# Optimization experiments

Hardware: AMD Instinct MI355X
Metric: run time of the kernel (lower is better)

## Reference

```python
import jax, jax.numpy as jnp
import numpy as np

DIM = 2048
H = 16
KV_RANK = 512
NOPE = 128
ROPE_D = 64
VD = 128
QK = NOPE + ROPE_D  # 192
SCALE = QK ** -0.5
B, S = 2, 2048
EPS = 1e-5


def _rope(x, start_pos):
    # x: (b, s, h, d) or (b, s, d); rotate along last dim, positions along axis 1
    s = x.shape[1]
    d = x.shape[-1]
    half = d // 2
    inv_freq = 1.0 / (10000.0 ** (jnp.arange(half, dtype=jnp.float32) * (2.0 / d)))
    pos = jnp.arange(start_pos, start_pos + s, dtype=jnp.float32)
    ang = pos[:, None] * inv_freq[None, :]  # (s, half)
    cos, sin = jnp.cos(ang), jnp.sin(ang)
    if x.ndim == 4:
        cos, sin = cos[None, :, None, :], sin[None, :, None, :]
    else:
        cos, sin = cos[None, :, :], sin[None, :, :]
    x1, x2 = x[..., :half], x[..., half:]
    return jnp.concatenate([x1 * cos - x2 * sin, x2 * cos + x1 * sin], axis=-1).astype(x.dtype)


def _layernorm(x, w, b):
    mu = jnp.mean(x, axis=-1, keepdims=True)
    var = jnp.mean(jnp.square(x - mu), axis=-1, keepdims=True)
    return (x - mu) * jax.lax.rsqrt(var + EPS) * w + b


def setup_inputs() -> dict:
    key = jax.random.key(0)
    ks = jax.random.split(key, 6)
    std = 0.02
    x = jax.random.normal(ks[0], (B, S, DIM), dtype=jnp.float32)
    wq = jax.random.normal(ks[1], (H * QK, DIM), dtype=jnp.float32) * std
    wkv_a = jax.random.normal(ks[2], (KV_RANK + ROPE_D, DIM), dtype=jnp.float32) * std
    wkv_b = jax.random.normal(ks[3], (H * (NOPE + VD), KV_RANK), dtype=jnp.float32) * std
    wo = jax.random.normal(ks[4], (DIM, H * VD), dtype=jnp.float32) * std
    kv_norm_w = jnp.ones((KV_RANK,), dtype=jnp.float32)
    kv_norm_b = jnp.zeros((KV_RANK,), dtype=jnp.float32)
    return {"x": x, "wq": wq, "wkv_a": wkv_a, "kv_norm_w": kv_norm_w,
            "kv_norm_b": kv_norm_b, "wkv_b": wkv_b, "wo": wo, "start_pos": 0}


def reference(x, wq, wkv_a, kv_norm_w, kv_norm_b, wkv_b, wo, start_pos):
    b, s, _ = x.shape
    # query projection: (b,s,H,QK)
    q = (x @ wq.T).reshape(b, s, H, QK)
    q_nope, q_pe = q[..., :NOPE], q[..., NOPE:]
    q_pe = _rope(q_pe, start_pos)
    # compressed kv + rope key
    kv_all = x @ wkv_a.T                      # (b,s,KV_RANK+ROPE_D)
    kv, k_pe = kv_all[..., :KV_RANK], kv_all[..., KV_RANK:]
    k_pe = _rope(k_pe, start_pos)             # (b,s,ROPE_D)
    kvn = _layernorm(kv, kv_norm_w, kv_norm_b)  # (b,s,KV_RANK)
    # absorb path: expand compressed kv through per-head wkv_b blocks
    w = wkv_b.reshape(H, NOPE + VD, KV_RANK)
    k_nope = jnp.einsum('btc,hdc->bthd', kvn, w[:, :NOPE])   # (b,t,H,NOPE)
    v = jnp.einsum('btc,hdc->bthd', kvn, w[:, NOPE:])        # (b,t,H,VD)
    q_full = jnp.concatenate([q_nope, q_pe], axis=-1)        # (b,s,H,QK)
    k_full = jnp.concatenate(
        [k_nope, jnp.broadcast_to(k_pe[:, :, None, :], (b, s, H, ROPE_D))], axis=-1)
    scores = jnp.einsum('bshd,bthd->bhst', q_full, k_full) * SCALE
    causal = jnp.tril(jnp.ones((s, s), dtype=bool))
    scores = jnp.where(causal[None, None], scores, jnp.float32(-1e30))
    attn = jax.nn.softmax(scores, axis=-1)
    out = jnp.einsum('bhst,bthd->bshd', attn, v).reshape(b, s, H * VD)
    return out @ wo.T
```

## Files before the change

kernel.cpp:

```cpp
#include <hip/hip_runtime.h>
#include <hip/hip_bf16.h>
#include <math.h>

typedef __bf16 bf16_t;
typedef __bf16 bf16x2 __attribute__((ext_vector_type(2)));
typedef __bf16 bf16x4 __attribute__((ext_vector_type(4)));
typedef __bf16 bf16x8 __attribute__((ext_vector_type(8)));
typedef float f32x4 __attribute__((ext_vector_type(4)));

#define SEQ 2048
#define MLA_SCALE 0.07216878364870322f
#define LN_EPS 1e-5f

__device__ __forceinline__ void gload_lds16(const bf16_t* g, bf16_t* l) {
    __builtin_amdgcn_global_load_lds(
        (const __attribute__((address_space(1))) uint32_t*)(const void*)g,
        (__attribute__((address_space(3))) uint32_t*)(void*)l, 16, 0, 0);
}

__device__ __forceinline__ void xcd_map(int bid, int total, int nbn,
                                        int& bm, int& bn) {
    int per = total >> 3;
    int cbm = per / nbn;
    int xcd = bid & 7, s = bid >> 3;
    int q = s / nbn;
    bm = xcd * cbm + q;
    bn = s - q * nbn;
}

#define CVT_N0 2097152
#define CVT_N1 1572864
#define CVT_N2 294912
#define CVT_N3 524288
#define CVT_N4 1048576
#define CVT_TOT (CVT_N0 + CVT_N1 + CVT_N2 + CVT_N3 + CVT_N4)

__global__ __launch_bounds__(256)
void cvt_all(const float* __restrict__ x, const float* __restrict__ wq,
             const float* __restrict__ wa, const float* __restrict__ wb,
             const float* __restrict__ wo, bf16_t* __restrict__ xb,
             bf16_t* __restrict__ wqb, bf16_t* __restrict__ wab,
             bf16_t* __restrict__ wbb, bf16_t* __restrict__ wob) {
    for (int i = blockIdx.x * 256 + threadIdx.x; i < CVT_TOT; i += gridDim.x * 256) {
        const float* src; bf16_t* dst; int off = i;
        if (i < CVT_N0) { src = x; dst = xb; }
        else if (i < CVT_N0 + CVT_N1) { src = wq; dst = wqb; off = i - CVT_N0; }
        else if (i < CVT_N0 + CVT_N1 + CVT_N2) { src = wa; dst = wab; off = i - CVT_N0 - CVT_N1; }
        else if (i < CVT_N0 + CVT_N1 + CVT_N2 + CVT_N3) { src = wb; dst = wbb; off = i - CVT_N0 - CVT_N1 - CVT_N2; }
        else { src = wo; dst = wob; off = i - CVT_N0 - CVT_N1 - CVT_N2 - CVT_N3; }
        float4 v = ((const float4*)src)[off];
        bf16x4 p = { (bf16_t)v.x, (bf16_t)v.y, (bf16_t)v.z, (bf16_t)v.w };
        ((bf16x4*)dst)[off] = p;
    }
}

#define G256_PHASE(TAU, KS, MH, HTO, MAT, WAITV)                               \
{                                                                              \
    const int slot_ = (2 * (TAU) + (KS)) & 3;                                  \
    bf16x8 af_[4];                                                             \
    {                                                                          \
        const bf16_t* ab_ = As + slot_ * 8192 +                                \
                            (wm2 * 128 + (MH) * 64 + lr) * 32 + rdcol;         \
        _Pragma("unroll")                                                      \
        for (int f = 0; f < 4; ++f) af_[f] = *(const bf16x8*)(ab_ + f * 512);  \
    }                                                                          \
    if ((MH) == 0) {                                                           \
        const bf16_t* bb_ = Bs + slot_ * 8192 + (wn2 * 64 + lr) * 32 + rdcol;  \
        _Pragma("unroll")                                                      \
        for (int f = 0; f < 4; ++f) bq[f] = *(const bf16x8*)(bb_ + f * 512);   \
    }                                                                          \
    if ((MAT) == 0) stageA(2 * T + 3 + (HTO)); else stageB(2 * T + 3 + (HTO)); \
    __builtin_amdgcn_s_barrier();                                              \
    asm volatile("" ::: "memory");                                             \
    __builtin_amdgcn_s_setprio(1);                                             \
    _Pragma("unroll")                                                          \
    for (int f = 0; f < 4; ++f)                                                \
        _Pragma("unroll")                                                      \
        for (int n = 0; n < 4; ++n)                                            \
            acc[(MH) * 4 + f][n] = __builtin_amdgcn_mfma_f32_16x16x32_bf16(    \
                af_[f], bq[n], acc[(MH) * 4 + f][n], 0, 0, 0);                 \
    __builtin_amdgcn_s_setprio(0);                                             \
    asm volatile("" ::: "memory");                                             \
    if (WAITV) asm volatile("s_waitcnt vmcnt(8)" ::: "memory");                \
    __builtin_amdgcn_s_barrier();                                              \
}

template<int MODE>
__global__ __launch_bounds__(512, 2)
void gemm256(const bf16_t* __restrict__ A, const bf16_t* __restrict__ B,
             float* __restrict__ C, bf16_t* __restrict__ out0,
             bf16_t* __restrict__ out1, int N, int K, int total, int nbn) {
    __shared__ __attribute__((aligned(16))) bf16_t As[32768];
    __shared__ __attribute__((aligned(16))) bf16_t Bs[32768];
    __shared__ __attribute__((aligned(16))) bf16_t Ds[8192];

    const int tid = threadIdx.x;
    const int lane = tid & 63, w = tid >> 6;
    const int lr = lane & 15, kh = lane >> 4;
    const int wm2 = w >> 2, wn2 = w & 3;
    int bm, bn;
    xcd_map(blockIdx.x, total, nbn, bm, bn);
    const int NT = K >> 6;

    const int rdcol = 8 * (kh ^ ((lr >> 1) & 3));
    const int strow = (w << 5) + (lane >> 2);
    const int scol = 8 * ((lane & 3) ^ ((lane >> 3) & 3));

    f32x4 acc[8][4];
    #pragma unroll
    for (int i = 0; i < 8; ++i)
        #pragma unroll
        for (int j = 0; j < 4; ++j) acc[i][j] = 0.0f;

    auto stageA = [&](int ht) {
        int hs = (ht < 2 * NT) ? ht : (2 * NT - 1);
        int tau = hs >> 1, kap = hs & 1;
        const bf16_t* g = A + (size_t)(bm * 256 + strow) * K + tau * 64 + kap * 32 + scol;
        bf16_t* l = (ht < 2 * NT) ? (As + (ht & 3) * 8192 + w * 1024) : (Ds + w * 1024);
        gload_lds16(g, l);
        gload_lds16(g + (size_t)16 * K, l + 512);
    };
    auto stageB = [&](int ht) {
        int hs = (ht < 2 * NT) ? ht : (2 * NT - 1);
        int tau = hs >> 1, kap = hs & 1;
        const bf16_t* g = B + (size_t)(bn * 256 + strow) * K + tau * 64 + kap * 32 + scol;
        bf16_t* l = (ht < 2 * NT) ? (Bs + (ht & 3) * 8192 + w * 1024) : (Ds + w * 1024);
        gload_lds16(g, l);
        gload_lds16(g + (size_t)16 * K, l + 512);
    };

    stageA(0); stageB(0); stageA(1); stageB(1); stageA(2); stageB(2);
    asm volatile("s_waitcnt vmcnt(8)" ::: "memory");
    __builtin_amdgcn_s_barrier();

    for (int it = 0; it < (NT >> 1); ++it) {
        const int T = 2 * it;
        bf16x8 bq[4];
        G256_PHASE(T,     0, 0, 0, 0, 0)
        G256_PHASE(T,     0, 1, 0, 1, 1)
        G256_PHASE(T,     1, 0, 1, 0, 0)
        G256_PHASE(T,     1, 1, 1, 1, 1)
        G256_PHASE(T + 1, 0, 0, 2, 0, 0)
        G256_PHASE(T + 1, 0, 1, 2, 1, 1)
        G256_PHASE(T + 1, 1, 0, 3, 0, 0)
        G256_PHASE(T + 1, 1, 1, 3, 1, 1)
    }

    const int rg = kh * 4;
    if (MODE == 0) {
        #pragma unroll
        for (int mf = 0; mf < 8; ++mf)
            #pragma unroll
            for (int nf = 0; nf < 4; ++nf) {
                size_t row0 = (size_t)(bm * 256 + wm2 * 128 + mf * 16 + rg);
                int col = bn * 256 + wn2 * 64 + nf * 16 + lr;
                #pragma unroll
                for (int rr = 0; rr < 4; ++rr)
                    C[(row0 + rr) * N + col] = acc[mf][nf][rr];
            }
    } else if (MODE == 1) {
        const int h = bn;
        #pragma unroll
        for (int mf = 0; mf < 8; ++mf)
            #pragma unroll
            for (int nf = 0; nf < 4; ++nf) {
                int d = wn2 * 64 + nf * 16 + lr;
                int trow = bm * 256 + wm2 * 128 + mf * 16 + rg;
                int b = trow >> 11, t = trow & 2047;
                if (d < 128) {
                    bf16_t* p = out0 + ((size_t)(b * 16 + h) * SEQ + t) * 192 + d;
                    #pragma unroll
                    for (int rr = 0; rr < 4; ++rr)
                        p[rr * 192] = (bf16_t)acc[mf][nf][rr];
                } else {
                    bf16x4 pv = { (bf16_t)acc[mf][nf][0], (bf16_t)acc[mf][nf][1],
                                  (bf16_t)acc[mf][nf][2], (bf16_t)acc[mf][nf][3] };
                    *(bf16x4*)(out1 + ((size_t)(b * 16 + h) * 128 + (d - 128)) * SEQ + t) = pv;
                }
            }
    } else {
        #pragma unroll
        for (int mf = 0; mf < 8; ++mf)
            #pragma unroll
            for (int nf = 0; nf < 4; ++nf) {
                int n = bn * 256 + wn2 * 64 + nf * 16 + lr;
                int h = n / 192, d = n - h * 192;
                int trow = bm * 256 + wm2 * 128 + mf * 16 + rg;
                int b = trow >> 11, t = trow & 2047;
                bf16_t* p = out0 + ((size_t)(b * 16 + h) * SEQ + t) * 192 + d;
                #pragma unroll
                for (int rr = 0; rr < 4; ++rr)
                    p[rr * 192] = (bf16_t)acc[mf][nf][rr];
            }
    }
}

__global__ __launch_bounds__(256)
void gemm_nt(const bf16_t* __restrict__ A, const bf16_t* __restrict__ B,
             float* __restrict__ C, int M, int N, int K, int total, int nbn) {
    __shared__ bf16_t As[4096], Bs[4096];
    int bm, bn;
    xcd_map(blockIdx.x, total, nbn, bm, bn);

    const int tid = threadIdx.x;
    const int lane = tid & 63, w = tid >> 6;
    const int lr = lane & 15, kh = lane >> 4;
    const int wm = (w >> 1) * 64, wn = (w & 1) * 64;
    const int subrow = lane >> 2;
    const int colel = (lane & 3) * 8;

    f32x4 acc[4][4];
    #pragma unroll
    for (int i = 0; i < 4; ++i)
        #pragma unroll
        for (int j = 0; j < 4; ++j) acc[i][j] = 0.0f;

    const int rA = bm * 128 + 32 * w + subrow;
    const int rB = bn * 128 + 32 * w + subrow;
    const int rb1 = (rB < N) ? rB : (N - 1);
    const int rb2 = (rB + 16 < N) ? (rB + 16) : (N - 1);

    for (int kt = 0; kt < K; kt += 32) {
        __syncthreads();
        gload_lds16(A + (size_t)rA * K + kt + colel,        As + (2 * w) * 512);
        gload_lds16(A + (size_t)(rA + 16) * K + kt + colel, As + (2 * w + 1) * 512);
        gload_lds16(B + (size_t)rb1 * K + kt + colel,       Bs + (2 * w) * 512);
        gload_lds16(B + (size_t)rb2 * K + kt + colel,       Bs + (2 * w + 1) * 512);
        __syncthreads();
        bf16x8 af[4], bfr[4];
        #pragma unroll
        for (int im = 0; im < 4; ++im)
            af[im] = *(const bf16x8*)(As + (wm + im * 16 + lr) * 32 + kh * 8);
        #pragma unroll
        for (int jn = 0; jn < 4; ++jn)
            bfr[jn] = *(const bf16x8*)(Bs + (wn + jn * 16 + lr) * 32 + kh * 8);
        #pragma unroll
        for (int im = 0; im < 4; ++im)
            #pragma unroll
            for (int jn = 0; jn < 4; ++jn)
                acc[im][jn] = __builtin_amdgcn_mfma_f32_16x16x32_bf16(
                    af[im], bfr[jn], acc[im][jn], 0, 0, 0);
    }

    const int rg = kh * 4;
    #pragma unroll
    for (int im = 0; im < 4; ++im)
        #pragma unroll
        for (int jn = 0; jn < 4; ++jn) {
            int col = bn * 128 + wn + jn * 16 + lr;
            if (col >= N) continue;
            size_t rowb = (size_t)(bm * 128 + wm + im * 16 + rg);
            #pragma unroll
            for (int rr = 0; rr < 4; ++rr)
                C[(rowb + rr) * N + col] = acc[im][jn][rr];
        }
}

__global__ __launch_bounds__(256)
void rope_ln(const float* __restrict__ kv_all,
             const float* __restrict__ lnw, const float* __restrict__ lnb,
             bf16_t* __restrict__ kvnb, bf16_t* __restrict__ kpack,
             float2* __restrict__ rope_cs, const int* __restrict__ start_pos) {
    const int m = blockIdx.x;
    const int tid = threadIdx.x;
    const int b = m >> 11, t = m & 2047;
    const float pos = (float)(start_pos[0] + t);
    __shared__ float red[8];
    __shared__ float stats[2];
    __shared__ float kbuf[64];

    const float* kvrow = kv_all + (size_t)m * 576;
    float v0 = kvrow[tid], v1 = kvrow[tid + 256];
    float ssum = v0 + v1, ssq = v0 * v0 + v1 * v1;
    for (int off = 32; off > 0; off >>= 1) {
        ssum += __shfl_down(ssum, off);
        ssq  += __shfl_down(ssq, off);
    }
    const int lane = tid & 63, wid = tid >> 6;
    if (lane == 0) { red[wid] = ssum; red[4 + wid] = ssq; }
    __syncthreads();
    if (tid == 0) {
        float ts = red[0] + red[1] + red[2] + red[3];
        float tq = red[4] + red[5] + red[6] + red[7];
        float mu = ts * (1.0f / 512.0f);
        float var = tq * (1.0f / 512.0f) - mu * mu;
        stats[0] = mu;
        stats[1] = rsqrtf(var + LN_EPS);
    }
    if (tid < 32) {
        int j = tid;
        float inv = expf(-(float)j * 0.2878231366242554f);
        float ang = pos * inv;
        float c = cosf(ang), sn = sinf(ang);
        float x1 = kvrow[512 + j], x2 = kvrow[544 + j];
        kbuf[j]      = x1 * c - x2 * sn;
        kbuf[32 + j] = x2 * c + x1 * sn;
        if (b == 0) rope_cs[t * 32 + j] = make_float2(c, sn);
    }
    __syncthreads();
    float mu = stats[0], rstd = stats[1];
    kvnb[(size_t)m * 512 + tid]       = (bf16_t)((v0 - mu) * rstd * lnw[tid] + lnb[tid]);
    kvnb[(size_t)m * 512 + tid + 256] = (bf16_t)((v1 - mu) * rstd * lnw[tid + 256] + lnb[tid + 256]);

    {
        int hh = tid >> 4, j4 = (tid & 15) * 4;
        bf16x4 pk = { (bf16_t)kbuf[j4], (bf16_t)kbuf[j4 + 1],
                      (bf16_t)kbuf[j4 + 2], (bf16_t)kbuf[j4 + 3] };
        *(bf16x4*)(kpack + ((size_t)(b * 16 + hh) * SEQ + t) * 192 + 128 + j4) = pk;
    }
}

__global__ __launch_bounds__(256, 2)
void attn_mfma(const bf16_t* __restrict__ qb, const bf16_t* __restrict__ kpack,
               const bf16_t* __restrict__ vt, const float2* __restrict__ rope_cs,
               bf16_t* __restrict__ ao) {
    __shared__ bf16_t Ks[2][64 * 192];
    __shared__ bf16_t Vts[128 * 64];
    __shared__ bf16_t Pls[4 * 16 * 64];

    const int bid = blockIdx.x;
    const int xcd = bid & 7, s = bid >> 3;
    const int g = xcd * 4 + (s >> 4);
    const int bx = s & 15;
    const int h = g & 15, b = g >> 4;

    const int tid = threadIdx.x;
    const int lane = tid & 63, w = tid >> 6;
    const int lr = lane & 15, kh = lane >> 4;
    const int lr7 = lr & 7;
    const int e0 = kh ^ lr7;
    const int e1 = (4 + kh) ^ lr7;
    const size_t bS = (size_t)b * SEQ;
    const bf16_t* kbase = kpack + (size_t)(b * 16 + h) * SEQ * 192;
    const bf16_t* vbase = vt + (size_t)(b * 16 + h) * 128 * SEQ;

    int kgo_[6], klo_[6], vgo_[4], vlo_[4], vco_[4];
    #pragma unroll
    for (int i = 0; i < 6; ++i) {
        int c = tid + 256 * i;
        int row = c / 24, slot = c % 24;
        kgo_[i] = row * 192 + slot * 8;
        klo_[i] = row * 192 + ((slot & 24) | ((slot ^ row) & 7)) * 8;
    }
    #pragma unroll
    for (int i = 0; i < 4; ++i) {
        int c = tid + 256 * i;
        int row = c >> 3, slot = c & 7;
        vgo_[i] = row;
        vlo_[i] = row * 64 + (slot ^ (row & 7)) * 8;
        vco_[i] = slot;
    }

    for (int half = 0; half < 2; ++half) {
        const int qt = half ? bx : (31 - bx);
        const int q0 = qt * 64;
        const int myrow = q0 + w * 16;
        const int qabs = myrow + lr;

        bf16x8 qf[6];
        {
            const bf16_t* qrow = qb + ((size_t)(b * 16 + h) * SEQ + qabs) * 192;
            #pragma unroll
            for (int ks = 0; ks < 6; ++ks)
                qf[ks] = *(const bf16x8*)(qrow + ks * 32 + kh * 8);
            const float2* csp = rope_cs + (size_t)qabs * 32 + kh * 8;
            #pragma unroll
            for (int i = 0; i < 8; ++i) {
                float2 cs = csp[i];
                float x1 = (float)qf[4][i], x2 = (float)qf[5][i];
                qf[4][i] = (bf16_t)(x1 * cs.x - x2 * cs.y);
                qf[5][i] = (bf16_t)(x2 * cs.x + x1 * cs.y);
            }
        }

        f32x4 O[8];
        #pragma unroll
        for (int i = 0; i < 8; ++i) O[i] = 0.0f;
        float m_r = -1e30f, l_r = 0.0f;

        bf16x8 rkw[6], rkl[6], rv[4];
        {
            bf16x8 rk0[6];
            #pragma unroll
            for (int i = 0; i < 6; ++i)
                rk0[i] = *(const bf16x8*)(kbase + kgo_[i]);
            #pragma unroll
            for (int i = 0; i < 6; ++i)
                *(bf16x8*)(Ks[0] + klo_[i]) = rk0[i];
        }
        {
            const int t1 = (qt > 0 ? 1 : 0) * 64;
            #pragma unroll
            for (int i = 0; i < 6; ++i)
                rkw[i] = *(const bf16x8*)(kbase + (size_t)t1 * 192 + kgo_[i]);
            #pragma unroll
            for (int i = 0; i < 4; ++i)
                rv[i] = *(const bf16x8*)(vbase + (size_t)vgo_[i] * SEQ + vco_[i] * 8);
        }
        __syncthreads();

        for (int kt = 0; kt <= qt; ++kt) {
            const int cur = kt & 1;
            const bf16_t* ksc = Ks[cur];
            bf16_t* ksn = Ks[cur ^ 1];

            if (kt < qt) {
                #pragma unroll
                for (int i = 0; i < 6; ++i)
                    *(bf16x8*)(ksn + klo_[i]) = rkw[i];
            }
            {
                const int tl = (kt + 2 <= qt ? kt + 2 : qt) * 64;
                #pragma unroll
                for (int i = 0; i < 6; ++i)
                    rkl[i] = *(const bf16x8*)(kbase + (size_t)tl * 192 + kgo_[i]);
            }

            f32x4 sacc[4];
            #pragma unroll
            for (int j = 0; j < 4; ++j) sacc[j] = 0.0f;
            __builtin_amdgcn_s_setprio(1);
            #pragma unroll
            for (int ks = 0; ks < 6; ++ks) {
                const int sw = (ks >> 1) * 64 + ((ks & 1) ? e1 : e0) * 8;
                #pragma unroll
                for (int j = 0; j < 4; ++j) {
                    bf16x8 kf = *(const bf16x8*)(ksc + (j * 16 + lr) * 192 + sw);
                    sacc[j] = __builtin_amdgcn_mfma_f32_16x16x32_bf16(kf, qf[ks], sacc[j], 0, 0, 0);
                }
            }
            __builtin_amdgcn_s_setprio(0);

            const int t0 = kt * 64;
            float p[16];
            if (kt == qt) {
                #pragma unroll
                for (int j = 0; j < 4; ++j)
                    #pragma unroll
                    for (int rr = 0; rr < 4; ++rr) {
                        int tabs = t0 + j * 16 + kh * 4 + rr;
                        p[j * 4 + rr] = (tabs > qabs) ? -1e30f : sacc[j][rr] * MLA_SCALE;
                    }
            } else {
                #pragma unroll
                for (int j = 0; j < 4; ++j)
                    #pragma unroll
                    for (int rr = 0; rr < 4; ++rr)
                        p[j * 4 + rr] = sacc[j][rr] * MLA_SCALE;
            }

            float mx = p[0];
            #pragma unroll
            for (int e = 1; e < 16; ++e) mx = fmaxf(mx, p[e]);
            mx = fmaxf(mx, __shfl_xor(mx, 16));
            mx = fmaxf(mx, __shfl_xor(mx, 32));

            if (!__all(mx <= m_r + 8.0f)) {
                float mnew = fmaxf(m_r, mx);
                float cr = __expf(m_r - mnew);
                l_r *= cr;
                m_r = mnew;
                float corr[4];
                #pragma unroll
                for (int rr = 0; rr < 4; ++rr)
                    corr[rr] = __shfl(cr, kh * 4 + rr);
                #pragma unroll
                for (int dt = 0; dt < 8; ++dt)
                    #pragma unroll
                    for (int rr = 0; rr < 4; ++rr)
                        O[dt][rr] *= corr[rr];
            }

            float ps = 0.0f;
            #pragma unroll
            for (int e = 0; e < 16; ++e) {
                p[e] = __expf(p[e] - m_r);
                ps += p[e];
            }
            ps += __shfl_xor(ps, 16);
            ps += __shfl_xor(ps, 32);
            l_r += ps;

            __syncthreads();
            #pragma unroll
            for (int i = 0; i < 4; ++i) *(bf16x8*)(Vts + vlo_[i]) = rv[i];
            {
                const int tv = (kt + 1 <= qt ? kt + 1 : qt) * 64;
                #pragma unroll
                for (int i = 0; i < 4; ++i)
                    rv[i] = *(const bf16x8*)(vbase + (size_t)vgo_[i] * SEQ + tv + vco_[i] * 8);
            }
            bf16_t* pw = Pls + (w * 16 + lr) * 64;
            const int f2 = kh >> 1, h4 = (kh & 1) * 4;
            #pragma unroll
            for (int j = 0; j < 4; ++j) {
                bf16x4 pp = { (bf16_t)p[j * 4], (bf16_t)p[j * 4 + 1],
                              (bf16_t)p[j * 4 + 2], (bf16_t)p[j * 4 + 3] };
                *(bf16x4*)(pw + ((2 * j + f2) ^ lr7) * 8 + h4) = pp;
            }
            __syncthreads();
            bf16x8 pa0 = *(const bf16x8*)(pw + e0 * 8);
            bf16x8 pa1 = *(const bf16x8*)(pw + e1 * 8);
            __builtin_amdgcn_s_setprio(1);
            #pragma unroll
            for (int dt = 0; dt < 8; ++dt) {
                bf16x8 b0 = *(const bf16x8*)(Vts + (dt * 16 + lr) * 64 + e0 * 8);
                O[dt] = __builtin_amdgcn_mfma_f32_16x16x32_bf16(pa0, b0, O[dt], 0, 0, 0);
                bf16x8 b1 = *(const bf16x8*)(Vts + (dt * 16 + lr) * 64 + e1 * 8);
                O[dt] = __builtin_amdgcn_mfma_f32_16x16x32_bf16(pa1, b1, O[dt], 0, 0, 0);
            }
            __builtin_amdgcn_s_setprio(0);
            #pragma unroll
            for (int i = 0; i < 6; ++i) rkw[i] = rkl[i];
        }

        float linv[4];
        #pragma unroll
        for (int rr = 0; rr < 4; ++rr)
            linv[rr] = 1.0f / __shfl(l_r, kh * 4 + rr);
        #pragma unroll
        for (int rr = 0; rr < 4; ++rr) {
            size_t rowb = (bS + myrow + kh * 4 + rr) * 2048 + h * 128;
            #pragma unroll
            for (int dt = 0; dt < 8; ++dt)
                ao[rowb + dt * 16 + lr] = (bf16_t)(O[dt][rr] * linv[rr]);
        }
        __syncthreads();
    }
}

extern "C" void kernel_launch(void* const* d_in, const int* in_sizes, int n_in,
                              void* d_out, int out_size, void* d_ws, size_t ws_size,
                              hipStream_t stream) {
    const float* x     = (const float*)d_in[0];
    const float* wq    = (const float*)d_in[1];
    const float* wkv_a = (const float*)d_in[2];
    const float* lnw   = (const float*)d_in[3];
    const float* lnb   = (const float*)d_in[4];
    const float* wkv_b = (const float*)d_in[5];
    const float* wo    = (const float*)d_in[6];
    const int* start_pos = (const int*)d_in[7];
    float* out = (float*)d_out;

    char* w8 = (char*)d_ws;
    bf16_t* xb   = (bf16_t*)(w8);
    bf16_t* wqb  = (bf16_t*)(w8 + 16777216);
    bf16_t* wab  = (bf16_t*)(w8 + 29360128);
    bf16_t* wbb  = (bf16_t*)(w8 + 31719424);
    bf16_t* wob  = (bf16_t*)(w8 + 35913728);
    bf16_t* kvnb = (bf16_t*)(w8 + 44302336);
    bf16_t* kpk  = (bf16_t*)(w8 + 48496640);
    bf16_t* vtb  = (bf16_t*)(w8 + 73662464);
    bf16_t* aob  = (bf16_t*)(w8 + 90439680);
    bf16_t* qbh  = (bf16_t*)(w8 + 107216896);
    float*  kva  = (float*)(w8 + 132382720);
    float2* rcs  = (float2*)(w8 + 141819904);

    cvt_all<<<2048, 256, 0, stream>>>(x, wq, wkv_a, wkv_b, wo, xb, wqb, wab, wbb, wob);

    gemm256<2><<<192, 512, 0, stream>>>(xb, wqb, nullptr, qbh, nullptr, 3072, 2048, 192, 12);
    gemm_nt<<<160, 256, 0, stream>>>(xb, wab, kva, 4096, 576, 2048, 160, 5);
    rope_ln<<<4096, 256, 0, stream>>>(kva, lnw, lnb, kvnb, kpk, rcs, start_pos);
    gemm256<1><<<256, 512, 0, stream>>>(kvnb, wbb, nullptr, kpk, vtb, 4096, 512, 256, 16);
    attn_mfma<<<512, 256, 0, stream>>>(qbh, kpk, vtb, rcs, aob);
    gemm_nt<<<512, 256, 0, stream>>>(aob, wob, out, 4096, 2048, 2048, 512, 16);
}
```

Baseline: 275.0 us.

## Double-buffer V tiles and pass P through register shuffles instead of LDS

The V tile now gets a double buffer in shared memory, prefetched two tiles ahead like K, so one barrier per iteration replaces the mid-loop barrier and store-to-LDS. The softmax probabilities P are packed to bf16 pairs and moved into MFMA A-operand layout with cross-lane shuffles instead of a write/read round trip through the Pls LDS buffer. This removes a __syncthreads and LDS traffic per KV tile. In exchange it adds more live registers (extra V prefetch registers) and about 16 shuffles per tile, which could pressure occupancy at launch bounds of 2 blocks.

```diff
diff --git a/kernel.cpp b/kernel.cpp
--- a/kernel.cpp
+++ b/kernel.cpp
@@ -7,6 +7,7 @@
 typedef __bf16 bf16x4 __attribute__((ext_vector_type(4)));
 typedef __bf16 bf16x8 __attribute__((ext_vector_type(8)));
 typedef float f32x4 __attribute__((ext_vector_type(4)));
+typedef uint32_t u32x4 __attribute__((ext_vector_type(4)));
 
 #define SEQ 2048
 #define MLA_SCALE 0.07216878364870322f
@@ -315,8 +316,7 @@
                const bf16_t* __restrict__ vt, const float2* __restrict__ rope_cs,
                bf16_t* __restrict__ ao) {
     __shared__ bf16_t Ks[2][64 * 192];
-    __shared__ bf16_t Vts[128 * 64];
-    __shared__ bf16_t Pls[4 * 16 * 64];
+    __shared__ bf16_t Vts[2][128 * 64];
 
     const int bid = blockIdx.x;
     const int xcd = bid & 7, s = bid >> 3;
@@ -351,6 +351,10 @@
         vco_[i] = slot;
     }
 
+    const int s1 = ((kh & 1) << 5) + lr;
+    const int s2 = s1 + 16;
+    const bool jhi = (kh >> 1) != 0;
+
     for (int half = 0; half < 2; ++half) {
         const int qt = half ? bx : (31 - bx);
         const int q0 = qt * 64;
@@ -378,15 +382,22 @@
         for (int i = 0; i < 8; ++i) O[i] = 0.0f;
         float m_r = -1e30f, l_r = 0.0f;
 
-        bf16x8 rkw[6], rkl[6], rv[4];
+        bf16x8 rkw[6], rkl[6], rvw[4], rvl[4];
         {
-            bf16x8 rk0[6];
+            bf16x8 t0[6];
             #pragma unroll
             for (int i = 0; i < 6; ++i)
-                rk0[i] = *(const bf16x8*)(kbase + kgo_[i]);
+                t0[i] = *(const bf16x8*)(kbase + kgo_[i]);
             #pragma unroll
             for (int i = 0; i < 6; ++i)
-                *(bf16x8*)(Ks[0] + klo_[i]) = rk0[i];
+                *(bf16x8*)(Ks[0] + klo_[i]) = t0[i];
+            bf16x8 t1[4];
+            #pragma unroll
+            for (int i = 0; i < 4; ++i)
+                t1[i] = *(const bf16x8*)(vbase + (size_t)vgo_[i] * SEQ + vco_[i] * 8);
+            #pragma unroll
+            for (int i = 0; i < 4; ++i)
+                *(bf16x8*)(Vts[0] + vlo_[i]) = t1[i];
         }
         {
             const int t1 = (qt > 0 ? 1 : 0) * 64;
@@ -395,25 +406,33 @@
                 rkw[i] = *(const bf16x8*)(kbase + (size_t)t1 * 192 + kgo_[i]);
             #pragma unroll
             for (int i = 0; i < 4; ++i)
-                rv[i] = *(const bf16x8*)(vbase + (size_t)vgo_[i] * SEQ + vco_[i] * 8);
+                rvl[i] = *(const bf16x8*)(vbase + (size_t)vgo_[i] * SEQ + t1 + vco_[i] * 8);
+            #pragma unroll
+            for (int i = 0; i < 4; ++i) rvw[i] = rvl[i];
         }
         __syncthreads();
 
         for (int kt = 0; kt <= qt; ++kt) {
             const int cur = kt & 1;
             const bf16_t* ksc = Ks[cur];
-            bf16_t* ksn = Ks[cur ^ 1];
+            const bf16_t* vsc = Vts[cur];
 
             if (kt < qt) {
                 #pragma unroll
                 for (int i = 0; i < 6; ++i)
-                    *(bf16x8*)(ksn + klo_[i]) = rkw[i];
+                    *(bf16x8*)(Ks[cur ^ 1] + klo_[i]) = rkw[i];
+                #pragma unroll
+                for (int i = 0; i < 4; ++i)
+                    *(bf16x8*)(Vts[cur ^ 1] + vlo_[i]) = rvw[i];
             }
             {
                 const int tl = (kt + 2 <= qt ? kt + 2 : qt) * 64;
                 #pragma unroll
                 for (int i = 0; i < 6; ++i)
                     rkl[i] = *(const bf16x8*)(kbase + (size_t)tl * 192 + kgo_[i]);
+                #pragma unroll
+                for (int i = 0; i < 4; ++i)
+                    rvl[i] = *(const bf16x8*)(vbase + (size_t)vgo_[i] * SEQ + tl + vco_[i] * 8);
             }
 
             f32x4 sacc[4];
@@ -481,37 +500,44 @@
             ps += __shfl_xor(ps, 32);
             l_r += ps;
 
+            auto pack2 = [](float a, float bb) {
+                bf16x2 t = { (bf16_t)a, (bf16_t)bb };
+                return __builtin_bit_cast(uint32_t, t);
+            };
+            uint32_t pk00 = pack2(p[0], p[1]),   pk01 = pack2(p[2], p[3]);
+            uint32_t pk10 = pack2(p[4], p[5]),   pk11 = pack2(p[6], p[7]);
+            uint32_t pk20 = pack2(p[8], p[9]),   pk21 = pack2(p[10], p[11]);
+            uint32_t pk30 = pack2(p[12], p[13]), pk31 = pack2(p[14], p[15]);
+            uint32_t q00 = __shfl(pk00, s1), q01 = __shfl(pk01, s1);
+            uint32_t q10 = __shfl(pk10, s1), q11 = __shfl(pk11, s1);
+            uint32_t r00 = __shfl(pk00, s2), r01 = __shfl(pk01, s2);
+            uint32_t r10 = __shfl(pk10, s2), r11 = __shfl(pk11, s2);
+            uint32_t q20 = __shfl(pk20, s1), q21 = __shfl(pk21, s1);
+            uint32_t q30 = __shfl(pk30, s1), q31 = __shfl(pk31, s1);
+            uint32_t r20 = __shfl(pk20, s2), r21 = __shfl(pk21, s2);
+            uint32_t r30 = __shfl(pk30, s2), r31 = __shfl(pk31, s2);
+            u32x4 ua = { jhi ? q10 : q00, jhi ? q11 : q01,
+                         jhi ? r10 : r00, jhi ? r11 : r01 };
+            u32x4 ub = { jhi ? q30 : q20, jhi ? q31 : q21,
+                         jhi ? r30 : r20, jhi ? r31 : r21 };
+            bf16x8 pa0 = __builtin_bit_cast(bf16x8, ua);
+            bf16x8 pa1 = __builtin_bit_cast(bf16x8, ub);
+
+            __builtin_amdgcn_s_setprio(1);
+            #pragma unroll
+            for (int dt = 0; dt < 8; ++dt) {
+                bf16x8 v0 = *(const bf16x8*)(vsc + (dt * 16 + lr) * 64 + e0 * 8);
+                O[dt] = __builtin_amdgcn_mfma_f32_16x16x32_bf16(pa0, v0, O[dt], 0, 0, 0);
+                bf16x8 v1 = *(const bf16x8*)(vsc + (dt * 16 + lr) * 64 + e1 * 8);
+                O[dt] = __builtin_amdgcn_mfma_f32_16x16x32_bf16(pa1, v1, O[dt], 0, 0, 0);
+            }
+            __builtin_amdgcn_s_setprio(0);
+
+            #pragma unroll
+            for (int i = 0; i < 6; ++i) rkw[i] = rkl[i];
+            #pragma unroll
+            for (int i = 0; i < 4; ++i) rvw[i] = rvl[i];
             __syncthreads();
-            #pragma unroll
-            for (int i = 0; i < 4; ++i) *(bf16x8*)(Vts + vlo_[i]) = rv[i];
-            {
-                const int tv = (kt + 1 <= qt ? kt + 1 : qt) * 64;
-                #pragma unroll
-                for (int i = 0; i < 4; ++i)
-                    rv[i] = *(const bf16x8*)(vbase + (size_t)vgo_[i] * SEQ + tv + vco_[i] * 8);
-            }
-            bf16_t* pw = Pls + (w * 16 + lr) * 64;
-            const int f2 = kh >> 1, h4 = (kh & 1) * 4;
-            #pragma unroll
-            for (int j = 0; j < 4; ++j) {
-                bf16x4 pp = { (bf16_t)p[j * 4], (bf16_t)p[j * 4 + 1],
-                              (bf16_t)p[j * 4 + 2], (bf16_t)p[j * 4 + 3] };
-                *(bf16x4*)(pw + ((2 * j + f2) ^ lr7) * 8 + h4) = pp;
-            }
-            __syncthreads();
-            bf16x8 pa0 = *(const bf16x8*)(pw + e0 * 8);
-            bf16x8 pa1 = *(const bf16x8*)(pw + e1 * 8);
-            __builtin_amdgcn_s_setprio(1);
-            #pragma unroll
-            for (int dt = 0; dt < 8; ++dt) {
-                bf16x8 b0 = *(const bf16x8*)(Vts + (dt * 16 + lr) * 64 + e0 * 8);
-                O[dt] = __builtin_amdgcn_mfma_f32_16x16x32_bf16(pa0, b0, O[dt], 0, 0, 0);
-                bf16x8 b1 = *(const bf16x8*)(Vts + (dt * 16 + lr) * 64 + e1 * 8);
-                O[dt] = __builtin_amdgcn_mfma_f32_16x16x32_bf16(pa1, b1, O[dt], 0, 0, 0);
-            }
-            __builtin_amdgcn_s_setprio(0);
-            #pragma unroll
-            for (int i = 0; i < 6; ++i) rkw[i] = rkl[i];
         }
 
         float linv[4];
```

Measured after the change: 279.8 us. Within noise of the previous version (+1.7%).
